# Performance work log

Hardware: AMD Instinct MI355X
Metric: run time of the kernel (lower is better)

## Reference

```python
import jax, jax.numpy as jnp
import numpy as np

NEG_SLOPE = 0.2  # PyG GATConv default negative_slope


def gat_conv(x, edge_index, W, a_src, a_dst, b):
    """PyG GATConv with add_self_loops=True, concat=False (mean over heads).
    x: [N, F_in]; W: [F_in, H*D]; a_src/a_dst: [H, D]; b: [D].
    Returns [N, D].
    """
    N = x.shape[0]
    H, D = a_src.shape
    xh = (x @ W).reshape(N, H, D)            # [N, H, D]
    loop = jnp.arange(N, dtype=edge_index.dtype)
    src = jnp.concatenate([edge_index[0], loop])  # [E+N]
    dst = jnp.concatenate([edge_index[1], loop])  # [E+N]
    # per-node attention logits
    asrc = jnp.einsum('nhd,hd->nh', xh, a_src)    # [N, H]
    adst = jnp.einsum('nhd,hd->nh', xh, a_dst)    # [N, H]
    e = asrc[src] + adst[dst]                      # [E+N, H]
    e = jnp.where(e > 0, e, NEG_SLOPE * e)         # LeakyReLU
    # softmax over incoming edges of each destination node
    emax = jax.ops.segment_max(e, dst, num_segments=N)   # [N, H]
    ex = jnp.exp(e - emax[dst])
    denom = jax.ops.segment_sum(ex, dst, num_segments=N) # [N, H]
    alpha = ex / denom[dst]                               # [E+N, H]
    # scatter-aggregate messages
    out = jax.ops.segment_sum(alpha[:, :, None] * xh[src], dst, num_segments=N)  # [N, H, D]
    return out.mean(axis=1) + b                           # concat=False -> mean heads


def setup_inputs() -> dict:
    key = jax.random.key(0)
    ks = jax.random.split(key, 10)
    N, F, D, C, H, E = 100000, 128, 32, 16, 8, 1600000
    s1 = 1.0 / np.sqrt(F)
    s2 = 1.0 / np.sqrt(D)
    return {
        'x': jax.random.normal(ks[0], (N, F), dtype=jnp.float32),
        'edge_index': jax.random.randint(ks[1], (2, E), 0, N, dtype=jnp.int32),
        'W1': jax.random.normal(ks[2], (F, H * D), dtype=jnp.float32) * s1,
        'a_src1': jax.random.normal(ks[3], (H, D), dtype=jnp.float32) * s2,
        'a_dst1': jax.random.normal(ks[4], (H, D), dtype=jnp.float32) * s2,
        'b1': jnp.zeros((D,), dtype=jnp.float32),
        'W2': jax.random.normal(ks[5], (D, H * C), dtype=jnp.float32) * s2,
        'a_src2': jax.random.normal(ks[6], (H, C), dtype=jnp.float32) * (1.0 / np.sqrt(C)),
        'a_dst2': jax.random.normal(ks[7], (H, C), dtype=jnp.float32) * (1.0 / np.sqrt(C)),
        'b2': jnp.zeros((C,), dtype=jnp.float32),
    }


def reference(x, edge_index, W1, a_src1, a_dst1, b1, W2, a_src2, a_dst2, b2):
    h = gat_conv(x, edge_index, W1, a_src1, a_dst1, b1)
    h = jax.nn.elu(h)                       # F.elu; Dropout(p=0.0) is identity
    logits = gat_conv(h, edge_index, W2, a_src2, a_dst2, b2)
    return (jax.nn.log_softmax(logits, axis=1), logits)
```

## Files before the change

kernel.cpp:

```cpp
#include <hip/hip_runtime.h>
#include <hip/hip_bf16.h>
#include <hip/hip_fp16.h>
#include <math.h>

#define LEAK 0.2f
#define BSTRIDE 64
#define NPB 128
#define CAPB 4096

typedef _Float16 f16;
typedef _Float16 f16x8 __attribute__((ext_vector_type(8)));
typedef float f32x2 __attribute__((ext_vector_type(2)));
typedef float f32x4 __attribute__((ext_vector_type(4)));

__global__ void transpose_w_k(const float* __restrict__ W, f16* __restrict__ Wt,
                              int K, int NC) {
  int idx = blockIdx.x * 256 + threadIdx.x;
  if (idx >= K * NC) return;
  int n = idx / K, k = idx - n * K;
  Wt[idx] = (f16)W[(size_t)k * NC + n];
}

__global__ __launch_bounds__(256) void binbuild_k(const uint2* __restrict__ recs,
                                                  const unsigned* __restrict__ binCnt,
                                                  unsigned* __restrict__ cnt,
                                                  unsigned* __restrict__ bucket, int N) {
  __shared__ unsigned lcnt[NPB];
  __shared__ unsigned lbkt[NPB * BSTRIDE];
  const int b = blockIdx.x;
  for (int i = threadIdx.x; i < NPB; i += 256) lcnt[i] = 0;
  __syncthreads();
  unsigned nrec = binCnt[b];
  nrec = nrec > CAPB ? CAPB : nrec;
  const unsigned r0 = (unsigned)b << 12;
  const unsigned r1 = r0 + nrec;
  for (unsigned p = r0 + threadIdx.x; p < r1; p += 256) {
    uint2 r = recs[p];
    unsigned dl = r.y & (NPB - 1);
    unsigned pos = atomicAdd(&lcnt[dl], 1u);
    if (pos < BSTRIDE) lbkt[(dl << 6) + pos] = r.x;
  }
  __syncthreads();
  const int n0 = b * NPB;
  const int nv = (N - n0) < NPB ? (N - n0) : NPB;
  for (int i = threadIdx.x; i < nv; i += 256) cnt[n0 + i] = lcnt[i];
  uint4* gb = (uint4*)(bucket + ((size_t)n0 << 6));
  const uint4* lb = (const uint4*)lbkt;
  const int lim = nv * (BSTRIDE / 4);
  for (int i = threadIdx.x; i < lim; i += 256) gb[i] = lb[i];
}

template <int K, int BN, int DH, bool FILL>
__global__ __launch_bounds__(256) void gemm_att_mfma_k(
    const float* __restrict__ A, const f16* __restrict__ Bt,
    unsigned char* __restrict__ Cout, const float* __restrict__ a_src,
    const float* __restrict__ a_dst, float* __restrict__ asrc,
    float* __restrict__ adst, int M, int NC,
    const int* __restrict__ ei, int E, int Nn,
    unsigned* __restrict__ binCnt, unsigned long long* __restrict__ recs,
    int NB) {
  constexpr int CH = K / 8;
  constexpr int CT = BN / 16;
  constexpr int KT = K / 32;
  constexpr int LDSB = (BN * K * 2) > (64 * BN) ? (BN * K * 2) : (64 * BN);
  __shared__ __align__(16) unsigned char smem[LDSB];
  f16* Bs = (f16*)smem;
  unsigned char* stage = smem;
  const int tid = threadIdx.x;
  const int row0 = blockIdx.y * 64;
  const int col0 = blockIdx.x * BN;

#pragma unroll
  for (int it = 0; it < (BN * CH) / 256; ++it) {
    int idx = it * 256 + tid;
    int n = idx / CH, c = idx - n * CH;
    f16x8 h = *(const f16x8*)(Bt + (size_t)(col0 + n) * K + c * 8);
    *(f16x8*)&Bs[n * K + (((c + n) & (CH - 1)) << 3)] = h;
  }

  const int wv = tid >> 6;
  const int lane = tid & 63;
  const int l16 = lane & 15;
  const int l4 = lane >> 4;

  const int arow = row0 + wv * 16 + l16;
  const bool aok = arow < M;
  f16x8 afrag[KT];
#pragma unroll
  for (int kt = 0; kt < KT; ++kt) {
    float4 v0 = make_float4(0.f, 0.f, 0.f, 0.f), v1 = v0;
    if (aok) {
      const float* gp = A + (size_t)arow * K + (kt * 4 + l4) * 8;
      v0 = *(const float4*)gp;
      v1 = *(const float4*)(gp + 4);
    }
    afrag[kt] = {(f16)v0.x, (f16)v0.y, (f16)v0.z, (f16)v0.w,
                 (f16)v1.x, (f16)v1.y, (f16)v1.z, (f16)v1.w};
  }
  __syncthreads();

  f32x4 acc[CT];
#pragma unroll
  for (int ct = 0; ct < CT; ++ct) acc[ct] = (f32x4){0.f, 0.f, 0.f, 0.f};

#pragma unroll
  for (int kt = 0; kt < KT; ++kt) {
    int aj = kt * 4 + l4;
#pragma unroll
    for (int ct = 0; ct < CT; ++ct) {
      int br = ct * 16 + l16;
      f16x8 bv = *(const f16x8*)&Bs[br * K + (((aj + br) & (CH - 1)) << 3)];
      acc[ct] = __builtin_amdgcn_mfma_f32_16x16x32_f16(afrag[kt], bv, acc[ct], 0, 0, 0);
    }
  }

  constexpr int HPB = BN / DH;
  constexpr int CTH = DH / 16;
  float ps[HPB][4], pd[HPB][4];
#pragma unroll
  for (int hl = 0; hl < HPB; ++hl)
#pragma unroll
    for (int r = 0; r < 4; ++r) { ps[hl][r] = 0.f; pd[hl][r] = 0.f; }

#pragma unroll
  for (int ct = 0; ct < CT; ++ct) {
    int col = col0 + ct * 16 + l16;
    float vs = a_src[col];
    float vd = a_dst[col];
    int hl = ct / CTH;
#pragma unroll
    for (int r = 0; r < 4; ++r) {
      ps[hl][r] += acc[ct][r] * vs;
      pd[hl][r] += acc[ct][r] * vd;
    }
  }

#pragma unroll
  for (int hl = 0; hl < HPB; ++hl) {
#pragma unroll
    for (int r = 0; r < 4; ++r) {
      float s = ps[hl][r], d = pd[hl][r];
#pragma unroll
      for (int m = 1; m < 16; m <<= 1) {
        s += __shfl_xor(s, m, 64);
        d += __shfl_xor(d, m, 64);
      }
      if (l16 == 0) {
        int grow = row0 + wv * 16 + l4 * 4 + r;
        int h = (col0 / DH) + hl;
        if (grow < M) {
          asrc[(size_t)grow * 8 + h] = s;
          adst[(size_t)grow * 8 + h] = d;
        }
      }
    }
  }

  __syncthreads();
  {
    const int j = lane & 3;
    const unsigned selAB = ((4u + j) << (8 * j)) | ((unsigned)j << (8 * (j ^ 1)));
    const unsigned selCD = ((4u + j) << (8 * (j ^ 2))) | ((unsigned)j << (8 * (j ^ 3)));
    const unsigned selMix =
        0x03020100u + (0x04040404u & ((j & 2) ? 0xFFFF0000u : 0x0000FFFFu));
    const int row = wv * 16 + l4 * 4 + j;
    const int colq = (l16 >> 2) * 4;
    const int swz = (row & 7) << 4;
#pragma unroll
    for (int ct = 0; ct < CT; ++ct) {
      unsigned wpk = (unsigned)__builtin_amdgcn_cvt_pk_fp8_f32(
          acc[ct][0], acc[ct][1], 0, false);
      wpk = (unsigned)__builtin_amdgcn_cvt_pk_fp8_f32(
          acc[ct][2], acc[ct][3], (int)wpk, true);
      unsigned Bx = (unsigned)__shfl_xor((int)wpk, 1, 64);
      unsigned Cx = (unsigned)__shfl_xor((int)wpk, 2, 64);
      unsigned Dx = (unsigned)__shfl_xor((int)wpk, 3, 64);
      unsigned P1 = __builtin_amdgcn_perm(wpk, Bx, selAB);
      unsigned P2 = __builtin_amdgcn_perm(Cx, Dx, selCD);
      unsigned ow = __builtin_amdgcn_perm(P1, P2, selMix);
      int colb = ct * 16 + colq;
      *(unsigned*)&stage[row * BN + (colb ^ swz)] = ow;
    }
  }
  __syncthreads();
  {
    constexpr int CPR = BN / 16;
#pragma unroll
    for (int i = 0; i < (64 * CPR) / 256; ++i) {
      int cid = i * 256 + tid;
      int row = cid / CPR, ch = cid - row * CPR;
      int grow = row0 + row;
      if (grow < M) {
        uint4 v = *(const uint4*)&stage[row * BN + ((ch * 16) ^ ((row & 7) << 4))];
        *(uint4*)(Cout + (size_t)grow * NC + col0 + ch * 16) = v;
      }
    }
  }

  if (FILL) {
    __syncthreads();
    unsigned* lh = (unsigned*)smem;
    unsigned* gb2 = ((unsigned*)smem) + 1024;
    const int chunk = (int)(blockIdx.y * gridDim.x + blockIdx.x);
    const int Mtot = E + Nn;
    const int base = chunk * 2048;
    if (base < Mtot) {
      for (int i = tid; i < NB; i += 256) lh[i] = 0;
      __syncthreads();
      int sr[8], dr[8];
#pragma unroll
      for (int j = 0; j < 8; ++j) {
        int p = base + j * 256 + tid;
        if (p < Mtot) {
          int ss, dd;
          if (p < E) {
            ss = ei[p];
            dd = ei[E + p];
          } else {
            ss = dd = p - E;
          }
          sr[j] = ss;
          dr[j] = dd;
          atomicAdd(&lh[dd >> 7], 1u);
        } else {
          dr[j] = -1;
          sr[j] = 0;
        }
      }
      __syncthreads();
      for (int i = tid; i < NB; i += 256) {
        unsigned c = lh[i];
        gb2[i] = c ? atomicAdd(&binCnt[i], c) : 0u;
        lh[i] = 0;
      }
      __syncthreads();
#pragma unroll
      for (int j = 0; j < 8; ++j) {
        if (dr[j] >= 0) {
          int b = dr[j] >> 7;
          unsigned pos = gb2[b] + atomicAdd(&lh[b], 1u);
          if (pos < CAPB) {
            unsigned long long rec =
                ((unsigned long long)(unsigned)dr[j] << 32) | (unsigned)sr[j];
            recs[((size_t)b << 12) + pos] = rec;
          }
        }
      }
    }
  }
}

__global__ __launch_bounds__(256) void aggregate1_k(const unsigned char* __restrict__ xh8,
                                                    const float* __restrict__ asrc,
                                                    const float* __restrict__ adst,
                                                    const unsigned* __restrict__ cnt,
                                                    const unsigned* __restrict__ bucket,
                                                    const float* __restrict__ b1,
                                                    float* __restrict__ hout, int N) {
  __shared__ float wlds[4][64][8];
  __shared__ unsigned slds[4][64];
  const int lane = threadIdx.x & 63;
  const int wv = threadIdx.x >> 6;
  const int n = blockIdx.x * 4 + wv;
  const int nn = n < N ? n : N - 1;
  int deg = (int)cnt[nn];
  deg = deg > BSTRIDE ? BSTRIDE : deg;
  unsigned sv = bucket[((size_t)nn << 6) + lane];
  if (lane >= deg) sv = 0;

  float w[8];
  if (lane < deg) {
    const float4* ap = (const float4*)(asrc + (size_t)sv * 8);
    const float4* bp = (const float4*)(adst + (size_t)nn * 8);
    float4 a0 = ap[0], a1 = ap[1];
    float4 b0 = bp[0], b1v = bp[1];
    float e[8] = {a0.x + b0.x, a0.y + b0.y, a0.z + b0.z, a0.w + b0.w,
                  a1.x + b1v.x, a1.y + b1v.y, a1.z + b1v.z, a1.w + b1v.w};
#pragma unroll
    for (int j = 0; j < 8; ++j) {
      float t = e[j];
      t = t > 0.f ? t : LEAK * t;
      w[j] = __expf(t);
    }
  } else {
#pragma unroll
    for (int j = 0; j < 8; ++j) w[j] = 0.f;
  }
  *(float4*)&wlds[wv][lane][0] = make_float4(w[0], w[1], w[2], w[3]);
  *(float4*)&wlds[wv][lane][4] = make_float4(w[4], w[5], w[6], w[7]);
  slds[wv][lane] = sv;
  __syncthreads();
  if (n >= N) return;

  const int sub = lane >> 5;
  const int sl = lane & 31;
  const int h = sl >> 2;
  const uint2* xw = (const uint2*)xh8;

  float a0 = 0.f, a1 = 0.f, a2 = 0.f, a3 = 0.f;
  float a4 = 0.f, a5 = 0.f, a6 = 0.f, a7 = 0.f;
  float dsum = 0.f;
#pragma unroll 4
  for (int i = 0; i < deg; i += 2) {
    float w8 = wlds[wv][i + sub][h];
    unsigned s = slds[wv][i + sub];
    uint2 b = xw[(size_t)s * 32 + sl];
    f32x2 p0 = __builtin_amdgcn_cvt_pk_f32_fp8(b.x, false);
    f32x2 p1 = __builtin_amdgcn_cvt_pk_f32_fp8(b.x, true);
    f32x2 p2 = __builtin_amdgcn_cvt_pk_f32_fp8(b.y, false);
    f32x2 p3 = __builtin_amdgcn_cvt_pk_f32_fp8(b.y, true);
    a0 += w8 * p0.x; a1 += w8 * p0.y; a2 += w8 * p1.x; a3 += w8 * p1.y;
    a4 += w8 * p2.x; a5 += w8 * p2.y; a6 += w8 * p3.x; a7 += w8 * p3.y;
    dsum += w8;
  }

  a0 += __shfl_xor(a0, 32, 64); a1 += __shfl_xor(a1, 32, 64);
  a2 += __shfl_xor(a2, 32, 64); a3 += __shfl_xor(a3, 32, 64);
  a4 += __shfl_xor(a4, 32, 64); a5 += __shfl_xor(a5, 32, 64);
  a6 += __shfl_xor(a6, 32, 64); a7 += __shfl_xor(a7, 32, 64);
  dsum += __shfl_xor(dsum, 32, 64);

  float rinv = 0.125f * __builtin_amdgcn_rcpf(dsum);
  a0 *= rinv; a1 *= rinv; a2 *= rinv; a3 *= rinv;
  a4 *= rinv; a5 *= rinv; a6 *= rinv; a7 *= rinv;

#pragma unroll
  for (int m = 16; m >= 4; m >>= 1) {
    a0 += __shfl_xor(a0, m, 64); a1 += __shfl_xor(a1, m, 64);
    a2 += __shfl_xor(a2, m, 64); a3 += __shfl_xor(a3, m, 64);
    a4 += __shfl_xor(a4, m, 64); a5 += __shfl_xor(a5, m, 64);
    a6 += __shfl_xor(a6, m, 64); a7 += __shfl_xor(a7, m, 64);
  }
  if (lane < 4) {
    int d = lane * 8;
    float4 bv0 = *(const float4*)(b1 + d);
    float4 bv1 = *(const float4*)(b1 + d + 4);
    float o0 = a0 + bv0.x, o1 = a1 + bv0.y, o2 = a2 + bv0.z, o3 = a3 + bv0.w;
    float o4 = a4 + bv1.x, o5 = a5 + bv1.y, o6 = a6 + bv1.z, o7 = a7 + bv1.w;
    o0 = o0 > 0.f ? o0 : expm1f(o0);
    o1 = o1 > 0.f ? o1 : expm1f(o1);
    o2 = o2 > 0.f ? o2 : expm1f(o2);
    o3 = o3 > 0.f ? o3 : expm1f(o3);
    o4 = o4 > 0.f ? o4 : expm1f(o4);
    o5 = o5 > 0.f ? o5 : expm1f(o5);
    o6 = o6 > 0.f ? o6 : expm1f(o6);
    o7 = o7 > 0.f ? o7 : expm1f(o7);
    *(float4*)(hout + (size_t)n * 32 + d) = make_float4(o0, o1, o2, o3);
    *(float4*)(hout + (size_t)n * 32 + d + 4) = make_float4(o4, o5, o6, o7);
  }
}

__global__ __launch_bounds__(256) void aggregate2_k(const unsigned char* __restrict__ xq,
                                                    const float* __restrict__ asrc,
                                                    const float* __restrict__ adst,
                                                    const unsigned* __restrict__ cnt,
                                                    const unsigned* __restrict__ bucket,
                                                    const float* __restrict__ b2,
                                                    float* __restrict__ out, int N) {
  __shared__ float wlds[4][64][8];
  __shared__ unsigned slds[4][64];
  const int lane = threadIdx.x & 63;
  const int wv = threadIdx.x >> 6;
  const int n = blockIdx.x * 4 + wv;
  const int nn = n < N ? n : N - 1;
  int deg = (int)cnt[nn];
  deg = deg > BSTRIDE ? BSTRIDE : deg;
  unsigned sv = __builtin_nontemporal_load(&bucket[((size_t)nn << 6) + lane]);
  if (lane >= deg) sv = 0;

  float w[8];
  if (lane < deg) {
    const float4* ap = (const float4*)(asrc + (size_t)sv * 8);
    const float4* bp = (const float4*)(adst + (size_t)nn * 8);
    float4 a0 = ap[0], a1 = ap[1];
    float4 b0 = bp[0], b1v = bp[1];
    float e[8] = {a0.x + b0.x, a0.y + b0.y, a0.z + b0.z, a0.w + b0.w,
                  a1.x + b1v.x, a1.y + b1v.y, a1.z + b1v.z, a1.w + b1v.w};
#pragma unroll
    for (int j = 0; j < 8; ++j) {
      float t = e[j];
      t = t > 0.f ? t : LEAK * t;
      w[j] = __expf(t);
    }
  } else {
#pragma unroll
    for (int j = 0; j < 8; ++j) w[j] = 0.f;
  }
  *(float4*)&wlds[wv][lane][0] = make_float4(w[0], w[1], w[2], w[3]);
  *(float4*)&wlds[wv][lane][4] = make_float4(w[4], w[5], w[6], w[7]);
  slds[wv][lane] = sv;
  __syncthreads();
  if (n >= N) return;

  const int sub = lane >> 5;
  const int sl = lane & 31;
  const int h = sl >> 2;
  const unsigned* xw = (const unsigned*)xq;

  float a0 = 0.f, a1 = 0.f, a2 = 0.f, a3 = 0.f;
  float dsum = 0.f;
#pragma unroll 4
  for (int i = 0; i < deg; i += 2) {
    float w8 = wlds[wv][i + sub][h];
    unsigned s = slds[wv][i + sub];
    unsigned b = xw[(size_t)s * 32 + sl];
    f32x2 p0 = __builtin_amdgcn_cvt_pk_f32_fp8(b, false);
    f32x2 p1 = __builtin_amdgcn_cvt_pk_f32_fp8(b, true);
    a0 += w8 * p0.x; a1 += w8 * p0.y; a2 += w8 * p1.x; a3 += w8 * p1.y;
    dsum += w8;
  }

  a0 += __shfl_xor(a0, 32, 64); a1 += __shfl_xor(a1, 32, 64);
  a2 += __shfl_xor(a2, 32, 64); a3 += __shfl_xor(a3, 32, 64);
  dsum += __shfl_xor(dsum, 32, 64);

  float rinv = 0.125f * __builtin_amdgcn_rcpf(dsum);
  a0 *= rinv; a1 *= rinv; a2 *= rinv; a3 *= rinv;

#pragma unroll
  for (int m = 16; m >= 4; m >>= 1) {
    a0 += __shfl_xor(a0, m, 64); a1 += __shfl_xor(a1, m, 64);
    a2 += __shfl_xor(a2, m, 64); a3 += __shfl_xor(a3, m, 64);
  }
  int c = (lane & 3) * 4;
  float4 bv = *(const float4*)(b2 + c);
  float l0 = a0 + bv.x, l1 = a1 + bv.y, l2 = a2 + bv.z, l3 = a3 + bv.w;

  float mx = fmaxf(fmaxf(l0, l1), fmaxf(l2, l3));
  mx = fmaxf(mx, __shfl_xor(mx, 1, 64));
  mx = fmaxf(mx, __shfl_xor(mx, 2, 64));
  float es = __expf(l0 - mx) + __expf(l1 - mx) + __expf(l2 - mx) + __expf(l3 - mx);
  es += __shfl_xor(es, 1, 64);
  es += __shfl_xor(es, 2, 64);
  float lse = logf(es) + mx;

  if (lane < 4) {
    f32x4 v0 = {l0 - lse, l1 - lse, l2 - lse, l3 - lse};
    f32x4 v1 = {l0, l1, l2, l3};
    __builtin_nontemporal_store(v0, (f32x4*)(out + (size_t)n * 16 + c));
    __builtin_nontemporal_store(v1, (f32x4*)(out + (size_t)N * 16 + (size_t)n * 16 + c));
  }
}

extern "C" void kernel_launch(void* const* d_in, const int* in_sizes, int n_in,
                              void* d_out, int out_size, void* d_ws, size_t ws_size,
                              hipStream_t stream) {
  const float* x      = (const float*)d_in[0];
  const int*   ei     = (const int*)d_in[1];
  const float* W1     = (const float*)d_in[2];
  const float* a_src1 = (const float*)d_in[3];
  const float* a_dst1 = (const float*)d_in[4];
  const float* b1     = (const float*)d_in[5];
  const float* W2     = (const float*)d_in[6];
  const float* a_src2 = (const float*)d_in[7];
  const float* a_dst2 = (const float*)d_in[8];
  const float* b2     = (const float*)d_in[9];

  const int N = in_sizes[0] / 128;
  const int E = in_sizes[1] / 2;
  const int Mtot = E + N;
  const int NB = (N + NPB - 1) / NPB;

  char* w = (char*)d_ws;
  size_t used = 0;
  auto alloc = [&](size_t bytes) -> void* {
    size_t aligned = (bytes + 255) & ~(size_t)255;
    void* p = w + used;
    used += aligned;
    return p;
  };
  unsigned char* xh1q = (unsigned char*)alloc((size_t)N * 256);
  unsigned char* xh2q = xh1q;
  float*    hbuf   = (float*)alloc((size_t)N * 32 * 4);
  float*    asrc   = (float*)alloc((size_t)N * 8 * 4);
  float*    adst   = (float*)alloc((size_t)N * 8 * 4);
  unsigned* cnt    = (unsigned*)alloc((size_t)N * 4);
  unsigned* bucket = (unsigned*)alloc((size_t)N * BSTRIDE * 4);
  f16*      w1t    = (f16*)alloc((size_t)128 * 256 * 2);
  f16*      w2t    = (f16*)alloc((size_t)32 * 128 * 2);
  unsigned long long* recs = (unsigned long long*)alloc((size_t)NB * CAPB * 8);
  unsigned* binCnt = (unsigned*)alloc((size_t)NB * 4);
  (void)ws_size;

  float* out = (float*)d_out;
  const int gy = (N + 63) / 64;

  hipMemsetAsync(binCnt, 0, (size_t)NB * 4, stream);
  transpose_w_k<<<(128 * 256 + 255) / 256, 256, 0, stream>>>(W1, w1t, 128, 256);
  transpose_w_k<<<(32 * 128 + 255) / 256, 256, 0, stream>>>(W2, w2t, 32, 128);

  gemm_att_mfma_k<128, 128, 32, true><<<dim3(2, gy), 256, 0, stream>>>(
      x, w1t, xh1q, a_src1, a_dst1, asrc, adst, N, 256,
      ei, E, N, binCnt, recs, NB);

  binbuild_k<<<NB, 256, 0, stream>>>((const uint2*)recs, binCnt, cnt, bucket, N);

  aggregate1_k<<<(N + 3) / 4, 256, 0, stream>>>(xh1q, asrc, adst, cnt, bucket, b1, hbuf, N);

  gemm_att_mfma_k<32, 128, 16, false><<<dim3(1, gy), 256, 0, stream>>>(
      hbuf, w2t, xh2q, a_src2, a_dst2, asrc, adst, N, 128,
      nullptr, 0, 0, nullptr, nullptr, 0);
  aggregate2_k<<<(N + 3) / 4, 256, 0, stream>>>(xh2q, asrc, adst, cnt, bucket, b2, out, N);
}
```

Before: 348.4 us.

## Fuse layer-2 projection and attention logits into layer-1 aggregation epilogue

The second-layer linear transform (h @ W2) and its source/destination attention logits are now computed directly in aggregate1's epilogue. Each wave shuffles the ELU'd hidden vector across lanes and multiplies it by W2, which every block stages in LDS. The fp8-quantized xh2 and separate asrc2/adst2 buffers are written there. This removes the fp32 hbuf round trip through memory, the W2 transpose kernel and the separate layer-2 GEMM launch. In exchange, every block reloads 16KB of W2 into LDS, and the extra LDS use may lower occupancy.

```diff
diff --git a/kernel.cpp b/kernel.cpp
--- a/kernel.cpp
+++ b/kernel.cpp
@@ -256,9 +256,16 @@
                                                     const unsigned* __restrict__ cnt,
                                                     const unsigned* __restrict__ bucket,
                                                     const float* __restrict__ b1,
-                                                    float* __restrict__ hout, int N) {
+                                                    const float* __restrict__ W2,
+                                                    const float* __restrict__ a_src2,
+                                                    const float* __restrict__ a_dst2,
+                                                    unsigned char* __restrict__ xh2q,
+                                                    float* __restrict__ asrc2o,
+                                                    float* __restrict__ adst2o,
+                                                    int N) {
   __shared__ float wlds[4][64][8];
   __shared__ unsigned slds[4][64];
+  __shared__ float W2s[32 * 128];
   const int lane = threadIdx.x & 63;
   const int wv = threadIdx.x >> 6;
   const int n = blockIdx.x * 4 + wv;
@@ -267,6 +274,9 @@
   deg = deg > BSTRIDE ? BSTRIDE : deg;
   unsigned sv = bucket[((size_t)nn << 6) + lane];
   if (lane >= deg) sv = 0;
+
+  for (int i = threadIdx.x; i < 1024; i += 256)
+    ((float4*)W2s)[i] = ((const float4*)W2)[i];
 
   float w[8];
   if (lane < deg) {
@@ -337,16 +347,50 @@
     float4 bv1 = *(const float4*)(b1 + d + 4);
     float o0 = a0 + bv0.x, o1 = a1 + bv0.y, o2 = a2 + bv0.z, o3 = a3 + bv0.w;
     float o4 = a4 + bv1.x, o5 = a5 + bv1.y, o6 = a6 + bv1.z, o7 = a7 + bv1.w;
-    o0 = o0 > 0.f ? o0 : expm1f(o0);
-    o1 = o1 > 0.f ? o1 : expm1f(o1);
-    o2 = o2 > 0.f ? o2 : expm1f(o2);
-    o3 = o3 > 0.f ? o3 : expm1f(o3);
-    o4 = o4 > 0.f ? o4 : expm1f(o4);
-    o5 = o5 > 0.f ? o5 : expm1f(o5);
-    o6 = o6 > 0.f ? o6 : expm1f(o6);
-    o7 = o7 > 0.f ? o7 : expm1f(o7);
-    *(float4*)(hout + (size_t)n * 32 + d) = make_float4(o0, o1, o2, o3);
-    *(float4*)(hout + (size_t)n * 32 + d + 4) = make_float4(o4, o5, o6, o7);
+    a0 = o0 > 0.f ? o0 : expm1f(o0);
+    a1 = o1 > 0.f ? o1 : expm1f(o1);
+    a2 = o2 > 0.f ? o2 : expm1f(o2);
+    a3 = o3 > 0.f ? o3 : expm1f(o3);
+    a4 = o4 > 0.f ? o4 : expm1f(o4);
+    a5 = o5 > 0.f ? o5 : expm1f(o5);
+    a6 = o6 > 0.f ? o6 : expm1f(o6);
+    a7 = o7 > 0.f ? o7 : expm1f(o7);
+  }
+
+  {
+    const float2* w2p = (const float2*)W2s;
+    float out0 = 0.f, out1 = 0.f;
+#pragma unroll
+    for (int q = 0; q < 4; ++q) {
+      float h0 = __shfl(a0, q, 64), h1 = __shfl(a1, q, 64);
+      float h2 = __shfl(a2, q, 64), h3 = __shfl(a3, q, 64);
+      float h4 = __shfl(a4, q, 64), h5 = __shfl(a5, q, 64);
+      float h6 = __shfl(a6, q, 64), h7 = __shfl(a7, q, 64);
+      float2 w0 = w2p[(q * 8 + 0) * 64 + lane];
+      float2 w1 = w2p[(q * 8 + 1) * 64 + lane];
+      float2 w2v = w2p[(q * 8 + 2) * 64 + lane];
+      float2 w3 = w2p[(q * 8 + 3) * 64 + lane];
+      float2 w4 = w2p[(q * 8 + 4) * 64 + lane];
+      float2 w5 = w2p[(q * 8 + 5) * 64 + lane];
+      float2 w6 = w2p[(q * 8 + 6) * 64 + lane];
+      float2 w7 = w2p[(q * 8 + 7) * 64 + lane];
+      out0 += h0 * w0.x + h1 * w1.x + h2 * w2v.x + h3 * w3.x +
+              h4 * w4.x + h5 * w5.x + h6 * w6.x + h7 * w7.x;
+      out1 += h0 * w0.y + h1 * w1.y + h2 * w2v.y + h3 * w3.y +
+              h4 * w4.y + h5 * w5.y + h6 * w6.y + h7 * w7.y;
+    }
+    const int c0 = lane * 2;
+    float ps2 = out0 * a_src2[c0] + out1 * a_src2[c0 + 1];
+    float pd2 = out0 * a_dst2[c0] + out1 * a_dst2[c0 + 1];
+    ps2 += __shfl_xor(ps2, 1, 64); pd2 += __shfl_xor(pd2, 1, 64);
+    ps2 += __shfl_xor(ps2, 2, 64); pd2 += __shfl_xor(pd2, 2, 64);
+    ps2 += __shfl_xor(ps2, 4, 64); pd2 += __shfl_xor(pd2, 4, 64);
+    int pk = __builtin_amdgcn_cvt_pk_fp8_f32(out0, out1, 0, false);
+    *(unsigned short*)(xh2q + (size_t)n * 128 + c0) = (unsigned short)(pk & 0xffff);
+    if ((lane & 7) == 0) {
+      asrc2o[(size_t)n * 8 + (lane >> 3)] = ps2;
+      adst2o[(size_t)n * 8 + (lane >> 3)] = pd2;
+    }
   }
 }
 
@@ -470,14 +514,14 @@
     return p;
   };
   unsigned char* xh1q = (unsigned char*)alloc((size_t)N * 256);
-  unsigned char* xh2q = xh1q;
-  float*    hbuf   = (float*)alloc((size_t)N * 32 * 4);
+  unsigned char* xh2q = (unsigned char*)alloc((size_t)N * 128);
   float*    asrc   = (float*)alloc((size_t)N * 8 * 4);
   float*    adst   = (float*)alloc((size_t)N * 8 * 4);
+  float*    asrc2  = (float*)alloc((size_t)N * 8 * 4);
+  float*    adst2  = (float*)alloc((size_t)N * 8 * 4);
   unsigned* cnt    = (unsigned*)alloc((size_t)N * 4);
   unsigned* bucket = (unsigned*)alloc((size_t)N * BSTRIDE * 4);
   f16*      w1t    = (f16*)alloc((size_t)128 * 256 * 2);
-  f16*      w2t    = (f16*)alloc((size_t)32 * 128 * 2);
   unsigned long long* recs = (unsigned long long*)alloc((size_t)NB * CAPB * 8);
   unsigned* binCnt = (unsigned*)alloc((size_t)NB * 4);
   (void)ws_size;
@@ -487,7 +531,6 @@
 
   hipMemsetAsync(binCnt, 0, (size_t)NB * 4, stream);
   transpose_w_k<<<(128 * 256 + 255) / 256, 256, 0, stream>>>(W1, w1t, 128, 256);
-  transpose_w_k<<<(32 * 128 + 255) / 256, 256, 0, stream>>>(W2, w2t, 32, 128);
 
   gemm_att_mfma_k<128, 128, 32, true><<<dim3(2, gy), 256, 0, stream>>>(
       x, w1t, xh1q, a_src1, a_dst1, asrc, adst, N, 256,
@@ -495,10 +538,9 @@
 
   binbuild_k<<<NB, 256, 0, stream>>>((const uint2*)recs, binCnt, cnt, bucket, N);
 
-  aggregate1_k<<<(N + 3) / 4, 256, 0, stream>>>(xh1q, asrc, adst, cnt, bucket, b1, hbuf, N);
-
-  gemm_att_mfma_k<32, 128, 16, false><<<dim3(1, gy), 256, 0, stream>>>(
-      hbuf, w2t, xh2q, a_src2, a_dst2, asrc, adst, N, 128,
-      nullptr, 0, 0, nullptr, nullptr, 0);
-  aggregate2_k<<<(N + 3) / 4, 256, 0, stream>>>(xh2q, asrc, adst, cnt, bucket, b2, out, N);
+  aggregate1_k<<<(N + 3) / 4, 256, 0, stream>>>(
+      xh1q, asrc, adst, cnt, bucket, b1, W2, a_src2, a_dst2,
+      xh2q, asrc2, adst2, N);
+
+  aggregate2_k<<<(N + 3) / 4, 256, 0, stream>>>(xh2q, asrc2, adst2, cnt, bucket, b2, out, N);
 }
```

Result: slower. 369.3 us (+6.0%).
